# Performance work log

Measured on AMD Instinct MI355X. Metric: run time of the kernel, lower is better.

The kernel has to match this reference:

```python
import jax, jax.numpy as jnp
import numpy as np

B, CIN, T, H, W = 4, 64, 8, 32, 32
COUT, AHID = 64, 16
HWF = H * W


def _conv2d(x, w, b):
    y = jax.lax.conv_general_dilated(x, w, (1, 1), [(1, 1), (1, 1)],
                                     dimension_numbers=("NCHW", "OIHW", "NCHW"))
    return y + b[None, :, None, None]


def _conv1x1(x, w, b):
    return jnp.einsum("bchw,oc->bohw", x, w) + b[None, :, None, None]


def setup_inputs():
    key = jax.random.key(0)
    ks = jax.random.split(key, 18)
    s = 0.05
    d = {}
    d["X"] = jax.random.normal(ks[0], (B, CIN, T, H, W), jnp.float32)
    d["conv_w"] = jax.random.normal(ks[1], (4 * COUT, CIN + COUT, 3, 3), jnp.float32) * s
    d["conv_b"] = jnp.zeros((4 * COUT,), jnp.float32)
    d["W_ci"] = jax.random.normal(ks[2], (COUT, H, W), jnp.float32) * s
    d["W_cf"] = jax.random.normal(ks[3], (COUT, H, W), jnp.float32) * s
    d["W_co"] = jax.random.normal(ks[4], (COUT, H, W), jnp.float32) * s
    d["q_w"] = jax.random.normal(ks[5], (AHID, COUT), jnp.float32) * s
    d["q_b"] = jnp.zeros((AHID,), jnp.float32)
    d["k_w"] = jax.random.normal(ks[6], (AHID, COUT), jnp.float32) * s
    d["k_b"] = jnp.zeros((AHID,), jnp.float32)
    d["k2_w"] = jax.random.normal(ks[7], (AHID, COUT), jnp.float32) * s
    d["k2_b"] = jnp.zeros((AHID,), jnp.float32)
    d["v_w"] = jax.random.normal(ks[8], (COUT, COUT), jnp.float32) * s
    d["v_b"] = jnp.zeros((COUT,), jnp.float32)
    d["v2_w"] = jax.random.normal(ks[9], (COUT, COUT), jnp.float32) * s
    d["v2_b"] = jnp.zeros((COUT,), jnp.float32)
    d["z_w"] = jax.random.normal(ks[10], (2 * COUT, 2 * COUT), jnp.float32) * s
    d["z_b"] = jnp.zeros((2 * COUT,), jnp.float32)
    d["m_w"] = jax.random.normal(ks[11], (3 * COUT, 3 * COUT), jnp.float32) * s
    d["m_b"] = jnp.zeros((3 * COUT,), jnp.float32)
    return d


def _forward(X, conv_w, conv_b, W_ci, W_cf, W_co, q_w, q_b, k_w, k_b, k2_w, k2_b,
             v_w, v_b, v2_w, v2_b, z_w, z_b, m_w, m_b):
    def step(carry, x_t):
        h, c, m = carry
        # ConvLSTM cell with peephole connections
        gates = _conv2d(jnp.concatenate([x_t, h], axis=1), conv_w, conv_b)
        i_c, f_c, g_c, o_c = jnp.split(gates, 4, axis=1)
        ig = jax.nn.sigmoid(i_c + W_ci * c)
        fg = jax.nn.sigmoid(f_c + W_cf * c)
        c_new = fg * c + ig * jnp.tanh(g_c)
        og = jax.nn.sigmoid(o_c + W_co * c_new)
        h_new = og * jnp.tanh(c_new)
        # Self-attention memory module (all projections are 1x1 convs)
        q = _conv1x1(h_new, q_w, q_b).reshape(B, AHID, HWF)
        kh = _conv1x1(h_new, k_w, k_b).reshape(B, AHID, HWF)
        vh = _conv1x1(h_new, v_w, v_b).reshape(B, COUT, HWF)
        km = _conv1x1(m, k2_w, k2_b).reshape(B, AHID, HWF)
        vm = _conv1x1(m, v2_w, v2_b).reshape(B, COUT, HWF)
        att_h = jax.nn.softmax(jnp.einsum("ban,bam->bnm", q, kh), axis=-1)  # (B,HW,HW)
        att_m = jax.nn.softmax(jnp.einsum("ban,bam->bnm", q, km), axis=-1)
        z_h = jnp.einsum("bnm,bcm->bcn", att_h, vh)  # (B,COUT,HW)
        z_m = jnp.einsum("bnm,bcm->bcn", att_m, vm)
        z = jnp.concatenate([z_h, z_m], axis=1).reshape(B, 2 * COUT, H, W)
        z = _conv1x1(z, z_w, z_b)
        comb = _conv1x1(jnp.concatenate([z, h_new], axis=1), m_w, m_b)
        mo, mg, mi = jnp.split(comb, 3, axis=1)
        gi = jax.nn.sigmoid(mi)
        m_new = (1.0 - gi) * m + gi * jnp.tanh(mg)
        h_out = jax.nn.sigmoid(mo) * m_new
        return (h_out, c_new, m_new), h_out

    zeros = jnp.zeros((B, COUT, H, W), X.dtype)
    Xs = jnp.moveaxis(X, 2, 0)  # (T, B, CIN, H, W)
    _, hs = jax.lax.scan(step, (zeros, zeros, zeros), Xs)
    return jnp.moveaxis(hs, 0, 2)  # (B, COUT, T, H, W)


def reference(X, conv_w, conv_b, W_ci, W_cf, W_co, q_w, q_b, k_w, k_b, k2_w, k2_b,
              v_w, v_b, v2_w, v2_b, z_w, z_b, m_w, m_b):
    return _forward(X, conv_w, conv_b, W_ci, W_cf, W_co, q_w, q_b, k_w, k_b,
                    k2_w, k2_b, v_w, v_b, v2_w, v2_b, z_w, z_b, m_w, m_b)
```

## Files before the change

### kernel.cpp

```cpp
#include <hip/hip_runtime.h>
#include <hip/hip_bf16.h>

typedef __hip_bfloat16 bf16;
typedef unsigned short ushort;
typedef __attribute__((ext_vector_type(8))) short short8v;
typedef __attribute__((ext_vector_type(4))) float float4v;

__device__ __forceinline__ float b2f(bf16 v){ return __bfloat162float(v); }
__device__ __forceinline__ float sigm(float x){ return 1.0f/(1.0f+__expf(-x)); }
__device__ __forceinline__ float tanhc(float x){
  x = fminf(15.0f, fmaxf(-15.0f, x));
  float e = __expf(2.0f*x);
  return (e-1.0f)/(e+1.0f);
}
__device__ __forceinline__ ushort f2bu(float f){
  bf16 h = __float2bfloat16(f); return *reinterpret_cast<ushort*>(&h);
}
__device__ __forceinline__ float bu2f(ushort u){
  return __uint_as_float(((unsigned)u)<<16);
}
__device__ __forceinline__ short8v ldfrag(const ushort* p){
  return *reinterpret_cast<const short8v*>(p);
}
__device__ __forceinline__ void glds16(const ushort* g, ushort* l){
  __builtin_amdgcn_global_load_lds(
    (const __attribute__((address_space(1))) unsigned int*)g,
    (__attribute__((address_space(3))) unsigned int*)l, 16, 0, 0);
}

#define WS_SMALL   0
#define WS_FLAG    262144
#define WS_ZROW    262160
#define WS_H       262208
#define WS_C       524352
#define WS_M       786496
#define WS_QB16    1310784
#define WS_KHB16   1376320
#define WS_KMB16   1441856
#define WS_VTH16   1507392
#define WS_VTM16   1638464
#define WS_MTH     1769536
#define WS_MTL     1900608
#define WS_HNTH    2031680
#define WS_HNTL    2162752
#define WS_ZW16H   2293824
#define WS_ZW16L   2302016
#define WS_MW16H   2310208
#define WS_MW16L   2328640
#define WS_WXAH    2347072
#define WS_WHAH    2420800
#define WS_WXAL    2494528
#define WS_WHAL    2568256
#define WS_XTHI    2641984
#define WS_XTLO    3690560
#define WS_HTHI    4739136
#define WS_HTLO    4870208
#define WS_PWH     5001280
#define WS_PWL     5006912
#define WS_GXG     5012544
#define WS_GXO     7109696
#define O_CB    0
#define O_WCI   256
#define O_WCF   65792
#define O_WCO   131328
#define O_QW    196864
#define O_QB    197888
#define O_KW    197904
#define O_KB    198928
#define O_K2W   198944
#define O_K2B   199968
#define O_VW    199984
#define O_VB    204080
#define O_V2W   204144
#define O_V2B   208240
#define O_ZW    208304
#define O_ZB    224688
#define O_MW    224816
#define O_MB    261680

__global__ void k_probe(const unsigned int* __restrict__ Xu, int* __restrict__ flag){
  __shared__ int cnt;
  if (threadIdx.x == 0) cnt = 0;
  __syncthreads();
  unsigned int u = Xu[threadIdx.x];
  float f = __uint_as_float((u & 0xffffu) << 16);
  int bad = (fabsf(f) <= 1e4f) ? 0 : 1;
  atomicAdd(&cnt, bad);
  __syncthreads();
  if (threadIdx.x == 0) *flag = (cnt > 16) ? 1 : 0;
}

struct P18 { const void* p[18]; };

__global__ __launch_bounds__(256) void k_wconv(P18 pk, const int* __restrict__ flagp,
                                               float* __restrict__ dst){
  const int ns[18]   = {256,65536,65536,65536,1024,16,1024,16,1024,16,
                        4096,64,4096,64,16384,128,36864,192};
  const int offs[18] = {O_CB,O_WCI,O_WCF,O_WCO,O_QW,O_QB,O_KW,O_KB,O_K2W,O_K2B,
                        O_VW,O_VB,O_V2W,O_V2B,O_ZW,O_ZB,O_MW,O_MB};
  int y = blockIdx.y;
  int n = ns[y];
  int flag = *flagp;
  const void* src = pk.p[y];
  for (int i = blockIdx.x*256 + threadIdx.x; i < n; i += gridDim.x*256){
    float v = flag ? ((const float*)src)[i] : b2f(((const bf16*)src)[i]);
    dst[offs[y] + i] = v;
  }
}

__global__ __launch_bounds__(256) void k_wtrans(float* __restrict__ ws){
  int i = blockIdx.x*256 + threadIdx.x;
  if (i < 16384){
    float f = ws[O_ZW + i];
    ushort h = f2bu(f);
    ((ushort*)(ws + WS_ZW16H))[i] = h;
    ((ushort*)(ws + WS_ZW16L))[i] = f2bu(f - bu2f(h));
  }
  if (i < 36864){
    float f = ws[O_MW + i];
    ushort h = f2bu(f);
    ((ushort*)(ws + WS_MW16H))[i] = h;
    ((ushort*)(ws + WS_MW16L))[i] = f2bu(f - bu2f(h));
  }
  if (i < 11264){
    int r = i >> 6, k = i & 63;
    float f;
    if (r < 16)       f = ws[O_QW  + r*64 + k];
    else if (r < 32)  f = ws[O_KW  + (r-16)*64 + k];
    else if (r < 48)  f = ws[O_K2W + (r-32)*64 + k];
    else if (r < 112) f = ws[O_VW  + (r-48)*64 + k];
    else              f = ws[O_V2W + (r-112)*64 + k];
    ushort h = f2bu(f);
    ((ushort*)(ws + WS_PWH))[i] = h;
    ((ushort*)(ws + WS_PWL))[i] = f2bu(f - bu2f(h));
  }
}

__global__ __launch_bounds__(256) void k_init(const void* __restrict__ conv_w,
                                              const int* __restrict__ flagp,
                                              float* __restrict__ ws){
  int i = blockIdx.x*256 + threadIdx.x;
  int flag = *flagp;
  if (i < 786432) ws[WS_H + i] = 0.0f;
  if (i < 32) ws[WS_ZROW + i] = 0.0f;
  if (i < 196608) ((unsigned*)(ws + WS_QB16))[i] = 0u;
  if (i < 294912){
    int ci = i & 127;
    int j = i >> 7;
    int mm = j & 255, p = j >> 8;
    int cc = mm >> 2, g = mm & 3;
    int si = ((g*64 + cc)*128 + ci)*9 + p;
    float f;
    ushort hi, lo = 0;
    if (flag){
      f = ((const float*)conv_w)[si];
      hi = f2bu(f);
      lo = f2bu(f - bu2f(hi));
    } else {
      hi = ((const ushort*)conv_w)[si];
    }
    if (ci < 64){
      int di = (j << 6) + ((((ci >> 3) ^ (mm & 7)) << 3) | (ci & 7));
      ((ushort*)(ws + WS_WXAH))[di] = hi;
      ((ushort*)(ws + WS_WXAL))[di] = lo;
    } else {
      int c2 = ci - 64;
      int di = (j << 6) + ((((c2 >> 3) ^ (mm & 7)) << 3) | (c2 & 7));
      ((ushort*)(ws + WS_WHAH))[di] = hi;
      ((ushort*)(ws + WS_WHAL))[di] = lo;
    }
  }
  if (i < 131072){
    ((unsigned*)(ws + WS_HTHI))[i] = 0u;
    ((unsigned*)(ws + WS_HTLO))[i] = 0u;
    ((unsigned*)(ws + WS_MTH))[i] = 0u;
    ((unsigned*)(ws + WS_MTL))[i] = 0u;
  }
}

__global__ __launch_bounds__(256) void k_xt(const void* __restrict__ Xraw,
                                            const int* __restrict__ flagp,
                                            float* __restrict__ ws){
  __shared__ ushort hi_s[64][66];
  __shared__ ushort lo_s[64][66];
  int pt = blockIdx.x, s = blockIdx.y;
  int b = s >> 3, t = s & 7;
  int flag = *flagp;
  int tid = threadIdx.x;
  for (int k = 0; k < 16; ++k){
    int idx = tid + k*256;
    int ci = idx >> 6, pxl = idx & 63;
    size_t si = ((size_t)(b*64 + ci)*8 + t)*1024 + pt*64 + pxl;
    if (flag){
      float f = ((const float*)Xraw)[si];
      ushort h = f2bu(f);
      hi_s[pxl][ci] = h;
      lo_s[pxl][ci] = f2bu(f - bu2f(h));
    } else {
      hi_s[pxl][ci] = ((const ushort*)Xraw)[si];
    }
  }
  __syncthreads();
  ushort* xh = (ushort*)(ws + WS_XTHI) + ((size_t)s*1024 + pt*64)*64;
  ushort* xl = (ushort*)(ws + WS_XTLO) + ((size_t)s*1024 + pt*64)*64;
  for (int k = 0; k < 16; ++k){
    int idx = tid + k*256;
    int pxl = idx >> 6, ci = idx & 63;
    xh[pxl*64 + ci] = hi_s[pxl][ci];
    if (flag) xl[pxl*64 + ci] = lo_s[pxl][ci];
  }
}

__global__ __launch_bounds__(512, 4) void k_convx(
  const int* __restrict__ flagp,
  const ushort* __restrict__ wxah, const ushort* __restrict__ wxal,
  const ushort* __restrict__ xt_hi, const ushort* __restrict__ xt_lo,
  float* __restrict__ gxg, ushort* __restrict__ gxo)
{
  __shared__ ushort xabuf[8192];
  __shared__ ushort xsm[54*136];
  int nt = blockIdx.x, mh = blockIdx.y, tb = blockIdx.z;
  int tid = threadIdx.x;
  int flag = *flagp;
  int ytile = nt >> 1, x0 = (nt & 1) * 16;
  const ushort* xb  = xt_hi + (size_t)tb*65536;
  const ushort* xlb = xt_lo + (size_t)tb*65536;
  int w = tid >> 6, lane = tid & 63, lr = lane & 15, lk = lane >> 4;
  const ushort* aw  = wxah + (size_t)(mh*128 + w*16)*64 + lane*8;
  const ushort* awl = wxal + (size_t)(mh*128 + w*16)*64 + lane*8;
  ushort* areg = xabuf + w*1024;

  const uint4 Z16 = make_uint4(0,0,0,0);
  for (int idx = tid; idx < 864; idx += 512){
    int slot = idx >> 4, c = idx & 15;
    int rr = slot / 18, xi = slot - rr*18;
    int gy = ytile - 1 + rr, gx2 = x0 - 1 + xi;
    bool valid = (gy >= 0) & (gy < 32) & (gx2 >= 0) & (gx2 < 32);
    int px = gy*32 + gx2;
    uint4 v = Z16;
    if (valid){
      if (c < 8)       v = *reinterpret_cast<const uint4*>(xb  + (size_t)px*64 + c*8);
      else if (flag)   v = *reinterpret_cast<const uint4*>(xlb + (size_t)px*64 + (c-8)*8);
    }
    *reinterpret_cast<uint4*>(&xsm[slot*136 + c*8]) = v;
  }
  __syncthreads();

  int px = nt*16 + lr;
  int sw = lr & 7;
  const int cx0 = ((lk ^ sw) << 3);
  const int cx1 = (((4+lk) ^ sw) << 3);
  float4v acc = {0.f,0.f,0.f,0.f};

  #pragma unroll 1
  for (int p = 0; p < 9; ++p){
    glds16(aw + (size_t)p*16384,       areg);
    glds16(aw + (size_t)p*16384 + 512, areg + 512);
    asm volatile("s_waitcnt vmcnt(0)" ::: "memory");
    __builtin_amdgcn_sched_barrier(0);
    short8v A0 = ldfrag(areg + lr*64 + cx0);
    short8v A1 = ldfrag(areg + lr*64 + cx1);
    int pinl = (p/3)*18 + lr + (p%3);
    const ushort* bl = &xsm[pinl*136 + lk*8];
    short8v BX0 = ldfrag(bl), BX1 = ldfrag(bl+32);
    acc = __builtin_amdgcn_mfma_f32_16x16x32_bf16(A0, BX0, acc, 0,0,0);
    acc = __builtin_amdgcn_mfma_f32_16x16x32_bf16(A1, BX1, acc, 0,0,0);
    if (flag){
      short8v BXl0 = ldfrag(bl+64), BXl1 = ldfrag(bl+96);
      acc = __builtin_amdgcn_mfma_f32_16x16x32_bf16(A0, BXl0, acc, 0,0,0);
      acc = __builtin_amdgcn_mfma_f32_16x16x32_bf16(A1, BXl1, acc, 0,0,0);
      asm volatile("s_waitcnt lgkmcnt(0)" ::: "memory");
      __builtin_amdgcn_sched_barrier(0);
      glds16(awl + (size_t)p*16384,       areg);
      glds16(awl + (size_t)p*16384 + 512, areg + 512);
      asm volatile("s_waitcnt vmcnt(0)" ::: "memory");
      __builtin_amdgcn_sched_barrier(0);
      short8v Al0 = ldfrag(areg + lr*64 + cx0);
      short8v Al1 = ldfrag(areg + lr*64 + cx1);
      acc = __builtin_amdgcn_mfma_f32_16x16x32_bf16(Al0, BX0, acc, 0,0,0);
      acc = __builtin_amdgcn_mfma_f32_16x16x32_bf16(Al1, BX1, acc, 0,0,0);
      asm volatile("s_waitcnt lgkmcnt(0)" ::: "memory");
      __builtin_amdgcn_sched_barrier(0);
    } else {
      asm volatile("s_waitcnt lgkmcnt(0)" ::: "memory");
      __builtin_amdgcn_sched_barrier(0);
    }
  }

  {
    int cc = mh*32 + w*4 + lk;
    gxg[((size_t)tb*64 + cc)*1024 + px] = acc[2];
    ushort* go = gxo + ((size_t)tb*192 + cc*3)*1024 + px;
    go[0]    = f2bu(acc[0]);
    go[1024] = f2bu(acc[1]);
    go[2048] = f2bu(acc[3]);
  }
}

__global__ __launch_bounds__(1024, 4) void k_convp(
  const int* __restrict__ flagp,
  const ushort* __restrict__ whah, const ushort* __restrict__ whal,
  const ushort* __restrict__ ht_hi, const ushort* __restrict__ ht_lo,
  const float* __restrict__ gxg, const ushort* __restrict__ gxo,
  const float* __restrict__ smalls, float* __restrict__ cst,
  const ushort* __restrict__ pwh, const ushort* __restrict__ pwl,
  const ushort* __restrict__ mth, const ushort* __restrict__ mtl,
  ushort* __restrict__ hnth, ushort* __restrict__ hntl,
  ushort* __restrict__ qb16, ushort* __restrict__ khb16, ushort* __restrict__ kmb16,
  ushort* __restrict__ vth16, ushort* __restrict__ vtm16, int t)
{
  __shared__ ushort albuf[16384];
  __shared__ ushort bsm[54*136];
  __shared__ ushort hbh[16*72];
  __shared__ ushort hbl[16*72];
  int nt = blockIdx.x, b = blockIdx.y;
  int tid = threadIdx.x;
  int flag = *flagp;
  int ytile = nt >> 1, x0 = (nt & 1) * 16;

  const ushort* hb  = ht_hi + (size_t)b*65536;
  const ushort* hlb = ht_lo + (size_t)b*65536;

  int w = tid >> 6, lane = tid & 63, lr = lane & 15, lk = lane >> 4;
  const ushort* aw  = whah + (size_t)(w*16)*64 + lane*8;
  const ushort* awl = whal + (size_t)(w*16)*64 + lane*8;
  ushort* areg = albuf + w*1024;

  if (!flag){
    glds16(aw, areg);
    glds16(aw + 512, areg + 512);
  }

  int px = nt*16 + lr;
  int cc = w*4 + lk;
  int tb = b*8 + t;
  const ushort* go = gxo + ((size_t)tb*192 + cc*3)*1024 + px;
  float a0 = bu2f(go[0]);
  float a1 = bu2f(go[1024]);
  float a3 = bu2f(go[2048]);
  float a2 = gxg[((size_t)tb*64 + cc)*1024 + px];

  const uint4 Z16 = make_uint4(0,0,0,0);
  if (tid < 864){
    int slot = tid >> 4, c = tid & 15;
    int rr = slot / 18, xi = slot - rr*18;
    int gy = ytile - 1 + rr, gx2 = x0 - 1 + xi;
    bool valid = (gy >= 0) & (gy < 32) & (gx2 >= 0) & (gx2 < 32);
    int hpx = gy*32 + gx2;
    uint4 v = Z16;
    if (valid){
      if (c < 8) v = *reinterpret_cast<const uint4*>(hb  + (size_t)hpx*64 + c*8);
      else       v = *reinterpret_cast<const uint4*>(hlb + (size_t)hpx*64 + (c-8)*8);
    }
    *reinterpret_cast<uint4*>(&bsm[slot*136 + c*8]) = v;
  }
  __syncthreads();

  const int sw = lr & 7;
  const int c2n = ((lk ^ sw) << 3);
  const int c3n = (((4+lk) ^ sw) << 3);

  float4v acc = {a0, a1, a2, a3};

  if (!flag){
    #pragma unroll
    for (int p = 0; p < 9; ++p){
      if (p > 0){
        asm volatile("s_waitcnt vmcnt(0)" ::: "memory");
        __builtin_amdgcn_sched_barrier(0);
      }
      short8v A2 = ldfrag(areg + lr*64 + c2n);
      short8v A3 = ldfrag(areg + lr*64 + c3n);
      if (p < 8){
        asm volatile("s_waitcnt lgkmcnt(0)" ::: "memory");
        __builtin_amdgcn_sched_barrier(0);
        glds16(aw + (size_t)(p+1)*16384,       areg);
        glds16(aw + (size_t)(p+1)*16384 + 512, areg + 512);
        __builtin_amdgcn_sched_barrier(0);
      }
      int pinl = (p/3)*18 + lr + (p%3);
      const ushort* bl = &bsm[pinl*136 + lk*8];
      short8v BH0 = ldfrag(bl),    BH1 = ldfrag(bl+32);
      short8v BL0 = ldfrag(bl+64), BL1 = ldfrag(bl+96);
      acc = __builtin_amdgcn_mfma_f32_16x16x32_bf16(A2, BH0, acc, 0,0,0);
      acc = __builtin_amdgcn_mfma_f32_16x16x32_bf16(A3, BH1, acc, 0,0,0);
      acc = __builtin_amdgcn_mfma_f32_16x16x32_bf16(A2, BL0, acc, 0,0,0);
      acc = __builtin_amdgcn_mfma_f32_16x16x32_bf16(A3, BL1, acc, 0,0,0);
    }
  } else {
    #pragma unroll 1
    for (int p = 0; p < 9; ++p){
      glds16(aw + (size_t)p*16384,       areg);
      glds16(aw + (size_t)p*16384 + 512, areg + 512);
      asm volatile("s_waitcnt vmcnt(0)" ::: "memory");
      __builtin_amdgcn_sched_barrier(0);
      short8v A2 = ldfrag(areg + lr*64 + c2n);
      short8v A3 = ldfrag(areg + lr*64 + c3n);
      asm volatile("s_waitcnt lgkmcnt(0)" ::: "memory");
      __builtin_amdgcn_sched_barrier(0);
      glds16(awl + (size_t)p*16384,       areg);
      glds16(awl + (size_t)p*16384 + 512, areg + 512);
      asm volatile("s_waitcnt vmcnt(0)" ::: "memory");
      __builtin_amdgcn_sched_barrier(0);
      short8v Al2 = ldfrag(areg + lr*64 + c2n);
      short8v Al3 = ldfrag(areg + lr*64 + c3n);
      asm volatile("s_waitcnt lgkmcnt(0)" ::: "memory");
      __builtin_amdgcn_sched_barrier(0);
      int pinl = (p/3)*18 + lr + (p%3);
      const ushort* bl = &bsm[pinl*136 + lk*8];
      short8v BH0 = ldfrag(bl),    BH1 = ldfrag(bl+32);
      short8v BL0 = ldfrag(bl+64), BL1 = ldfrag(bl+96);
      acc = __builtin_amdgcn_mfma_f32_16x16x32_bf16(A2, BH0, acc, 0,0,0);
      acc = __builtin_amdgcn_mfma_f32_16x16x32_bf16(A3, BH1, acc, 0,0,0);
      acc = __builtin_amdgcn_mfma_f32_16x16x32_bf16(A2, BL0, acc, 0,0,0);
      acc = __builtin_amdgcn_mfma_f32_16x16x32_bf16(A3, BL1, acc, 0,0,0);
      acc = __builtin_amdgcn_mfma_f32_16x16x32_bf16(Al2, BH0, acc, 0,0,0);
      acc = __builtin_amdgcn_mfma_f32_16x16x32_bf16(Al3, BH1, acc, 0,0,0);
    }
  }

  {
    int wi = cc*1024 + px;
    size_t sidx = ((size_t)(b*64 + cc))*1024 + px;
    float cprev = cst[sidx];
    float ic = acc[0] + smalls[O_CB + cc];
    float fc = acc[1] + smalls[O_CB + 64 + cc];
    float gc = acc[2] + smalls[O_CB + 128 + cc];
    float oc = acc[3] + smalls[O_CB + 192 + cc];
    float ig = sigm(ic + smalls[O_WCI + wi]*cprev);
    float fg = sigm(fc + smalls[O_WCF + wi]*cprev);
    float cnew = fg*cprev + ig*tanhc(gc);
    float og = sigm(oc + smalls[O_WCO + wi]*cnew);
    cst[sidx] = cnew;
    float hv = og*tanhc(cnew);
    ushort hh = f2bu(hv);
    ushort hl2 = f2bu(hv - bu2f(hh));
    hbh[lr*72 + cc] = hh;
    hbl[lr*72 + cc] = hl2;
  }
  __syncthreads();

  {
    int ppx = tid >> 6, ccx = tid & 63;
    size_t tix2 = ((size_t)b*1024 + nt*16 + ppx)*64 + ccx;
    hnth[tix2] = hbh[ppx*72 + ccx];
    hntl[tix2] = hbl[ppx*72 + ccx];
  }

  if (w < 11){
    int tt = w;
    const float4v Z4 = {0.f,0.f,0.f,0.f};
    bool srcm = (tt == 2) || (tt >= 7);
    short8v b0, b1, bl0, bl1;
    if (srcm){
      size_t bb = ((size_t)b*1024 + nt*16 + lr)*64 + lk*8;
      b0  = ldfrag(mth + bb);  b1  = ldfrag(mth + bb + 32);
      bl0 = ldfrag(mtl + bb);  bl1 = ldfrag(mtl + bb + 32);
    } else {
      b0  = ldfrag(&hbh[lr*72 + lk*8]);  b1  = ldfrag(&hbh[lr*72 + 32 + lk*8]);
      bl0 = ldfrag(&hbl[lr*72 + lk*8]);  bl1 = ldfrag(&hbl[lr*72 + 32 + lk*8]);
    }
    const ushort* ar = pwh + (size_t)(tt*16 + lr)*64 + lk*8;
    short8v pa0 = ldfrag(ar), pa1 = ldfrag(ar + 32);
    float4v d = Z4;
    d = __builtin_amdgcn_mfma_f32_16x16x32_bf16(pa0, b0,  d, 0,0,0);
    d = __builtin_amdgcn_mfma_f32_16x16x32_bf16(pa1, b1,  d, 0,0,0);
    d = __builtin_amdgcn_mfma_f32_16x16x32_bf16(pa0, bl0, d, 0,0,0);
    d = __builtin_amdgcn_mfma_f32_16x16x32_bf16(pa1, bl1, d, 0,0,0);
    if (flag){
      const ushort* arl = pwl + (size_t)(tt*16 + lr)*64 + lk*8;
      short8v pal0 = ldfrag(arl), pal1 = ldfrag(arl + 32);
      d = __builtin_amdgcn_mfma_f32_16x16x32_bf16(pal0, b0, d, 0,0,0);
      d = __builtin_amdgcn_mfma_f32_16x16x32_bf16(pal1, b1, d, 0,0,0);
    }
    int n = nt*16 + lr;
    int boff = (tt==0) ? O_QB : (tt==1) ? O_KB : (tt==2) ? O_K2B
             : (tt<7) ? (O_VB + (tt-3)*16) : (O_V2B + (tt-7)*16);
    if (tt < 3){
      ushort* base = (tt==0) ? qb16 : (tt==1) ? khb16 : kmb16;
      ushort u[4];
      #pragma unroll
      for (int q = 0; q < 4; ++q)
        u[q] = f2bu(d[q] + smalls[boff + lk*4 + q]);
      *reinterpret_cast<uint2*>(&base[((size_t)b*1024 + n)*32 + lk*4]) =
        make_uint2((unsigned)u[0] | ((unsigned)u[1]<<16),
                   (unsigned)u[2] | ((unsigned)u[3]<<16));
    } else {
      ushort* base = (tt<7) ? vth16 : vtm16;
      int cc0 = ((tt<7) ? (tt-3) : (tt-7))*16 + lk*4;
      #pragma unroll
      for (int q = 0; q < 4; ++q)
        base[((size_t)b*64 + cc0 + q)*1024 + n] = f2bu(d[q] + smalls[boff + lk*4 + q]);
    }
  }
}

__global__ __launch_bounds__(512) void k_fattz(
  const ushort* __restrict__ qb16, const ushort* __restrict__ khb16,
  const ushort* __restrict__ kmb16, const ushort* __restrict__ vth16,
  const ushort* __restrict__ vtm16,
  const ushort* __restrict__ hnth, const ushort* __restrict__ hntl,
  const float* __restrict__ smalls,
  const ushort* __restrict__ zw16h, const ushort* __restrict__ zw16l,
  const ushort* __restrict__ mw16h, const ushort* __restrict__ mw16l,
  const int* __restrict__ flagp,
  float* __restrict__ mst, ushort* __restrict__ mth, ushort* __restrict__ mtl,
  ushort* __restrict__ hth, ushort* __restrict__ htl,
  void* __restrict__ outraw, int t)
{
  __shared__ __align__(16) unsigned char poolA[34816];
  __shared__ __align__(16) ushort ztbh[16*136];
  __shared__ __align__(16) ushort ztbl[16*136];
  __shared__ float cb[192*17];
  __shared__ float ml[64*17];
  __shared__ float rs_s[2][4][16];

  ushort* es   = (ushort*)poolA;
  ushort* zbh  = (ushort*)poolA;
  ushort* zbl  = (ushort*)(poolA + 8704);
  float*  ho_s = (float*)poolA;
  float*  mn_s = (float*)(poolA + 4352);

  int nt = blockIdx.x, b = blockIdx.y;
  int n0 = nt*16;
  int tid = threadIdx.x;
  int w = tid >> 6, lane = tid & 63, lr = lane & 15, lk = lane >> 4;
  int br = w >> 2, wq = w & 3;
  int flag = *flagp;
  const float4v Z4 = {0.f,0.f,0.f,0.f};

  const ushort* kb = (br ? kmb16 : khb16) + (size_t)b*32768;
  const ushort* vt = (br ? vtm16 : vth16) + (size_t)b*65536;
  const ushort* qp = qb16 + (size_t)b*32768;

  for (int idx = tid; idx < 1024; idx += 512){
    int ch = idx >> 4, pp = idx & 15;
    ml[ch*17+pp] = mst[((size_t)b*64 + ch)*1024 + n0 + pp];
  }

  short8v qf = ldfrag(qp + (size_t)(n0 + lr)*32 + lk*8);

  float4v acc[2];
  acc[0]=Z4; acc[1]=Z4;
  float rsum = 0.f;

  #pragma unroll 1
  for (int mc = 0; mc < 4; ++mc){
    ushort* esb = es + (br*2 + (mc & 1))*4352;
    int mbase = mc*256 + wq*64;
    #pragma unroll
    for (int tau = 0; tau < 4; ++tau){
      short8v af = ldfrag(kb + (size_t)(mbase + tau*16 + lr)*32 + lk*8);
      float4v d = __builtin_amdgcn_mfma_f32_16x16x32_bf16(af, qf, Z4, 0,0,0);
      ushort u0 = f2bu(__expf(fminf(d[0], 60.f)));
      ushort u1 = f2bu(__expf(fminf(d[1], 60.f)));
      ushort u2 = f2bu(__expf(fminf(d[2], 60.f)));
      ushort u3 = f2bu(__expf(fminf(d[3], 60.f)));
      rsum += (bu2f(u0) + bu2f(u1)) + (bu2f(u2) + bu2f(u3));
      unsigned lo = (unsigned)u0 | ((unsigned)u1 << 16);
      unsigned hi = (unsigned)u2 | ((unsigned)u3 << 16);
      *reinterpret_cast<uint2*>(&esb[lr*272 + wq*64 + tau*16 + lk*4]) = make_uint2(lo, hi);
    }
    __syncthreads();
    #pragma unroll
    for (int ks = 0; ks < 8; ++ks){
      short8v av = ldfrag(vt + (size_t)(wq*16 + lr)*1024 + mc*256 + ks*32 + lk*8);
      short8v bv = ldfrag(&esb[lr*272 + ks*32 + lk*8]);
      acc[ks & 1] = __builtin_amdgcn_mfma_f32_16x16x32_bf16(av, bv, acc[ks & 1], 0,0,0);
    }
  }

  {
    float r = rsum;
    r += __shfl_xor(r, 16);
    r += __shfl_xor(r, 32);
    if (lane < 16) rs_s[br][wq][lr] = r;
  }
  __syncthreads();
  {
    float rinv = 1.0f / (rs_s[br][0][lr] + rs_s[br][1][lr] + rs_s[br][2][lr] + rs_s[br][3][lr]);
    int ch0 = br*64 + wq*16 + lk*4;
    ushort uh[4], ul[4];
    #pragma unroll
    for (int r = 0; r < 4; ++r){
      float z = (acc[0][r] + acc[1][r])*rinv;
      uh[r] = f2bu(z);
      ul[r] = f2bu(z - bu2f(uh[r]));
    }
    *reinterpret_cast<uint2*>(&zbh[lr*136 + ch0]) =
      make_uint2((unsigned)uh[0] | ((unsigned)uh[1]<<16), (unsigned)uh[2] | ((unsigned)uh[3]<<16));
    *reinterpret_cast<uint2*>(&zbl[lr*136 + ch0]) =
      make_uint2((unsigned)ul[0] | ((unsigned)ul[1]<<16), (unsigned)ul[2] | ((unsigned)ul[3]<<16));
  }
  __syncthreads();

  {
    float4v zacc = Z4;
    if (!flag){
      #pragma unroll
      for (int kf = 0; kf < 4; ++kf){
        short8v a  = ldfrag(zw16h + (size_t)(w*16 + lr)*128 + kf*32 + lk*8);
        short8v bh = ldfrag(&zbh[lr*136 + kf*32 + lk*8]);
        short8v bl = ldfrag(&zbl[lr*136 + kf*32 + lk*8]);
        zacc = __builtin_amdgcn_mfma_f32_16x16x32_bf16(a, bh, zacc, 0,0,0);
        zacc = __builtin_amdgcn_mfma_f32_16x16x32_bf16(a, bl, zacc, 0,0,0);
      }
    } else {
      #pragma unroll
      for (int kf = 0; kf < 4; ++kf){
        short8v a  = ldfrag(zw16h + (size_t)(w*16 + lr)*128 + kf*32 + lk*8);
        short8v al = ldfrag(zw16l + (size_t)(w*16 + lr)*128 + kf*32 + lk*8);
        short8v bh = ldfrag(&zbh[lr*136 + kf*32 + lk*8]);
        short8v bl = ldfrag(&zbl[lr*136 + kf*32 + lk*8]);
        zacc = __builtin_amdgcn_mfma_f32_16x16x32_bf16(a,  bh, zacc, 0,0,0);
        zacc = __builtin_amdgcn_mfma_f32_16x16x32_bf16(a,  bl, zacc, 0,0,0);
        zacc = __builtin_amdgcn_mfma_f32_16x16x32_bf16(al, bh, zacc, 0,0,0);
      }
    }
    int r0 = w*16 + lk*4;
    ushort th[4], tl[4];
    #pragma unroll
    for (int q = 0; q < 4; ++q){
      float ztv = zacc[q] + smalls[O_ZB + r0 + q];
      th[q] = f2bu(ztv);
      tl[q] = f2bu(ztv - bu2f(th[q]));
    }
    *reinterpret_cast<uint2*>(&ztbh[lr*136 + r0]) =
      make_uint2((unsigned)th[0] | ((unsigned)th[1]<<16), (unsigned)th[2] | ((unsigned)th[3]<<16));
    *reinterpret_cast<uint2*>(&ztbl[lr*136 + r0]) =
      make_uint2((unsigned)tl[0] | ((unsigned)tl[1]<<16), (unsigned)tl[2] | ((unsigned)tl[3]<<16));
  }
  __syncthreads();

  const ushort* hrow  = hnth + ((size_t)b*1024 + n0 + lr)*64;
  const ushort* hrowl = hntl + ((size_t)b*1024 + n0 + lr)*64;
  #pragma unroll
  for (int mi = 0; mi < 2; ++mi){
    if (mi == 1 && w >= 4) break;
    int mf = (mi == 0) ? w : (w + 8);
    float4v cacc = Z4;
    const ushort* arow  = mw16h + (size_t)(mf*16 + lr)*192;
    const ushort* arowl = mw16l + (size_t)(mf*16 + lr)*192;
    if (!flag){
      #pragma unroll
      for (int kf = 0; kf < 4; ++kf){
        short8v a  = ldfrag(arow + kf*32 + lk*8);
        short8v bh = ldfrag(&ztbh[lr*136 + kf*32 + lk*8]);
        short8v bl = ldfrag(&ztbl[lr*136 + kf*32 + lk*8]);
        cacc = __builtin_amdgcn_mfma_f32_16x16x32_bf16(a, bh, cacc, 0,0,0);
        cacc = __builtin_amdgcn_mfma_f32_16x16x32_bf16(a, bl, cacc, 0,0,0);
      }
      #pragma unroll
      for (int kf = 0; kf < 2; ++kf){
        short8v a  = ldfrag(arow + 128 + kf*32 + lk*8);
        short8v bh = ldfrag(hrow + kf*32 + lk*8);
        short8v bl = ldfrag(hrowl + kf*32 + lk*8);
        cacc = __builtin_amdgcn_mfma_f32_16x16x32_bf16(a, bh, cacc, 0,0,0);
        cacc = __builtin_amdgcn_mfma_f32_16x16x32_bf16(a, bl, cacc, 0,0,0);
      }
    } else {
      #pragma unroll
      for (int kf = 0; kf < 4; ++kf){
        short8v a  = ldfrag(arow + kf*32 + lk*8);
        short8v al = ldfrag(arowl + kf*32 + lk*8);
        short8v bh = ldfrag(&ztbh[lr*136 + kf*32 + lk*8]);
        short8v bl = ldfrag(&ztbl[lr*136 + kf*32 + lk*8]);
        cacc = __builtin_amdgcn_mfma_f32_16x16x32_bf16(a,  bh, cacc, 0,0,0);
        cacc = __builtin_amdgcn_mfma_f32_16x16x32_bf16(a,  bl, cacc, 0,0,0);
        cacc = __builtin_amdgcn_mfma_f32_16x16x32_bf16(al, bh, cacc, 0,0,0);
      }
      #pragma unroll
      for (int kf = 0; kf < 2; ++kf){
        short8v a  = ldfrag(arow + 128 + kf*32 + lk*8);
        short8v al = ldfrag(arowl + 128 + kf*32 + lk*8);
        short8v bh = ldfrag(hrow + kf*32 + lk*8);
        short8v bl = ldfrag(hrowl + kf*32 + lk*8);
        cacc = __builtin_amdgcn_mfma_f32_16x16x32_bf16(a,  bh, cacc, 0,0,0);
        cacc = __builtin_amdgcn_mfma_f32_16x16x32_bf16(a,  bl, cacc, 0,0,0);
        cacc = __builtin_amdgcn_mfma_f32_16x16x32_bf16(al, bh, cacc, 0,0,0);
      }
    }
    int r0 = mf*16 + lk*4;
    #pragma unroll
    for (int q = 0; q < 4; ++q)
      cb[(r0+q)*17 + lr] = cacc[q] + smalls[O_MB + r0 + q];
  }
  __syncthreads();

  {
    int px = tid >> 5, lr2 = tid & 31;
    #pragma unroll
    for (int j = 0; j < 2; ++j){
      int ch = lr2 + 32*j;
      float mo = cb[ch*17 + px];
      float mg = cb[(64+ch)*17 + px];
      float mi = cb[(128+ch)*17 + px];
      float mold = ml[ch*17 + px];
      float gi = sigm(mi);
      float mnew = (1.0f-gi)*mold + gi*tanhc(mg);
      float ho = sigm(mo)*mnew;
      ho_s[ch*17+px] = ho;
      mn_s[ch*17+px] = mnew;
    }
  }
  __syncthreads();
  for (int idx = tid; idx < 1024; idx += 512){
    int ch = idx >> 4, pp = idx & 15;
    int n = n0 + pp;
    size_t gidx = ((size_t)b*64 + ch)*1024 + n;
    mst[gidx] = mn_s[ch*17+pp];
    float ho = ho_s[ch*17+pp];
    size_t oidx = ((size_t)(b*64+ch)*8 + t)*1024 + n;
    if (flag) ((float*)outraw)[oidx] = ho;
    else      ((bf16*)outraw)[oidx] = __float2bfloat16(ho);
  }
  for (int idx = tid; idx < 1024; idx += 512){
    int pp = idx >> 6, ch = idx & 63;
    int n = n0 + pp;
    size_t tix = ((size_t)b*1024 + n)*64 + ch;
    float ho = ho_s[ch*17+pp];
    float mn = mn_s[ch*17+pp];
    ushort hb_ = f2bu(ho);
    hth[tix] = hb_;
    htl[tix] = f2bu(ho - bu2f(hb_));
    ushort mh_ = f2bu(mn);
    mth[tix] = mh_;
    mtl[tix] = f2bu(mn - bu2f(mh_));
  }
}

extern "C" void kernel_launch(void* const* d_in, const int* in_sizes, int n_in,
                              void* d_out, int out_size, void* d_ws, size_t ws_size,
                              hipStream_t stream)
{
  float* ws = (float*)d_ws;
  int* flag = (int*)(ws + WS_FLAG);
  float* c    = ws + WS_C;
  float* m    = ws + WS_M;
  float* gxg  = ws + WS_GXG;
  ushort* gxo   = (ushort*)(ws + WS_GXO);
  ushort* qb16  = (ushort*)(ws + WS_QB16);
  ushort* khb16 = (ushort*)(ws + WS_KHB16);
  ushort* kmb16 = (ushort*)(ws + WS_KMB16);
  ushort* vth16 = (ushort*)(ws + WS_VTH16);
  ushort* vtm16 = (ushort*)(ws + WS_VTM16);
  ushort* mth   = (ushort*)(ws + WS_MTH);
  ushort* mtl   = (ushort*)(ws + WS_MTL);
  ushort* hnth  = (ushort*)(ws + WS_HNTH);
  ushort* hntl  = (ushort*)(ws + WS_HNTL);
  ushort* zw16h = (ushort*)(ws + WS_ZW16H);
  ushort* zw16l = (ushort*)(ws + WS_ZW16L);
  ushort* mw16h = (ushort*)(ws + WS_MW16H);
  ushort* mw16l = (ushort*)(ws + WS_MW16L);
  ushort* wxah  = (ushort*)(ws + WS_WXAH);
  ushort* wxal  = (ushort*)(ws + WS_WXAL);
  ushort* whah  = (ushort*)(ws + WS_WHAH);
  ushort* whal  = (ushort*)(ws + WS_WHAL);
  ushort* xt_hi = (ushort*)(ws + WS_XTHI);
  ushort* xt_lo = (ushort*)(ws + WS_XTLO);
  ushort* ht_hi = (ushort*)(ws + WS_HTHI);
  ushort* ht_lo = (ushort*)(ws + WS_HTLO);
  ushort* pwh   = (ushort*)(ws + WS_PWH);
  ushort* pwl   = (ushort*)(ws + WS_PWL);

  k_probe<<<1, 256, 0, stream>>>((const unsigned int*)d_in[0], flag);
  P18 pk;
  for (int i = 0; i < 18; ++i) pk.p[i] = d_in[2 + i];
  k_wconv<<<dim3(64,18), 256, 0, stream>>>(pk, flag, ws);
  k_init<<<3072, 256, 0, stream>>>(d_in[1], flag, ws);
  k_xt<<<dim3(16,32), 256, 0, stream>>>(d_in[0], flag, ws);
  k_wtrans<<<144, 256, 0, stream>>>(ws);
  k_convx<<<dim3(64,2,32), 512, 0, stream>>>(flag, wxah, wxal, xt_hi, xt_lo, gxg, gxo);

  for (int t = 0; t < 8; ++t){
    k_convp<<<dim3(64,4), 1024, 0, stream>>>(flag, whah, whal, ht_hi, ht_lo,
                                             gxg, gxo, ws, c, pwh, pwl, mth, mtl,
                                             hnth, hntl, qb16, khb16, kmb16,
                                             vth16, vtm16, t);
    k_fattz<<<dim3(64,4), 512, 0, stream>>>(qb16, khb16, kmb16, vth16, vtm16,
                                            hnth, hntl, ws, zw16h, zw16l, mw16h, mw16l,
                                            flag, m, mth, mtl, ht_hi, ht_lo, d_out, t);
  }
  (void)in_sizes; (void)n_in; (void)out_size; (void)ws_size;
}
```

Measured before the change: 389.8 us.

## Split attention key range across two wave groups with 1024-thread fattz blocks

Doubles the fused attention/z/m kernel block size to 1024 threads. Each branch's key chunks are now split between two wave halves, and the partial PV accumulators are merged through shared memory. The 1x1 conv and epilogue loops are remapped so each thread handles a single element. The aim is more parallelism in a latency-bound grid of only 256 blocks. The cost is more LDS (the score buffer doubles, plus a cross-wave reduction buffer), an extra reduction step, and tighter register limits under the 1024-thread launch bounds.

```diff
diff --git a/kernel.cpp b/kernel.cpp
--- a/kernel.cpp
+++ b/kernel.cpp
@@ -495,7 +495,7 @@
   }
 }
 
-__global__ __launch_bounds__(512) void k_fattz(
+__global__ __launch_bounds__(1024) void k_fattz(
   const ushort* __restrict__ qb16, const ushort* __restrict__ khb16,
   const ushort* __restrict__ kmb16, const ushort* __restrict__ vth16,
   const ushort* __restrict__ vtm16,
@@ -508,12 +508,13 @@
   ushort* __restrict__ hth, ushort* __restrict__ htl,
   void* __restrict__ outraw, int t)
 {
-  __shared__ __align__(16) unsigned char poolA[34816];
+  __shared__ __align__(16) unsigned char poolA[69632];
   __shared__ __align__(16) ushort ztbh[16*136];
   __shared__ __align__(16) ushort ztbl[16*136];
   __shared__ float cb[192*17];
   __shared__ float ml[64*17];
-  __shared__ float rs_s[2][4][16];
+  __shared__ float rs_s[2][8][16];
+  __shared__ float accx[2*4*64*4];
 
   ushort* es   = (ushort*)poolA;
   ushort* zbh  = (ushort*)poolA;
@@ -525,7 +526,7 @@
   int n0 = nt*16;
   int tid = threadIdx.x;
   int w = tid >> 6, lane = tid & 63, lr = lane & 15, lk = lane >> 4;
-  int br = w >> 2, wq = w & 3;
+  int br = w >> 3, sub = w & 7, mh2 = sub >> 2, wq = sub & 3;
   int flag = *flagp;
   const float4v Z4 = {0.f,0.f,0.f,0.f};
 
@@ -533,8 +534,8 @@
   const ushort* vt = (br ? vtm16 : vth16) + (size_t)b*65536;
   const ushort* qp = qb16 + (size_t)b*32768;
 
-  for (int idx = tid; idx < 1024; idx += 512){
-    int ch = idx >> 4, pp = idx & 15;
+  {
+    int ch = tid >> 4, pp = tid & 15;
     ml[ch*17+pp] = mst[((size_t)b*64 + ch)*1024 + n0 + pp];
   }
 
@@ -545,8 +546,9 @@
   float rsum = 0.f;
 
   #pragma unroll 1
-  for (int mc = 0; mc < 4; ++mc){
-    ushort* esb = es + (br*2 + (mc & 1))*4352;
+  for (int mci = 0; mci < 2; ++mci){
+    int mc = mh2*2 + mci;
+    ushort* esb = es + (size_t)(br*4 + mc)*4352;
     int mbase = mc*256 + wq*64;
     #pragma unroll
     for (int tau = 0; tau < 4; ++tau){
@@ -574,16 +576,25 @@
     float r = rsum;
     r += __shfl_xor(r, 16);
     r += __shfl_xor(r, 32);
-    if (lane < 16) rs_s[br][wq][lr] = r;
-  }
-  __syncthreads();
-  {
-    float rinv = 1.0f / (rs_s[br][0][lr] + rs_s[br][1][lr] + rs_s[br][2][lr] + rs_s[br][3][lr]);
+    if (lane < 16) rs_s[br][sub][lr] = r;
+  }
+  if (mh2 == 1){
+    float* ax = accx + ((size_t)(br*4 + wq)*64 + lane)*4;
+    #pragma unroll
+    for (int r = 0; r < 4; ++r) ax[r] = acc[0][r] + acc[1][r];
+  }
+  __syncthreads();
+  if (mh2 == 0){
+    float rtot = 0.f;
+    #pragma unroll
+    for (int s2 = 0; s2 < 8; ++s2) rtot += rs_s[br][s2][lr];
+    float rinv = 1.0f / rtot;
+    const float* ax = accx + ((size_t)(br*4 + wq)*64 + lane)*4;
     int ch0 = br*64 + wq*16 + lk*4;
     ushort uh[4], ul[4];
     #pragma unroll
     for (int r = 0; r < 4; ++r){
-      float z = (acc[0][r] + acc[1][r])*rinv;
+      float z = (acc[0][r] + acc[1][r] + ax[r])*rinv;
       uh[r] = f2bu(z);
       ul[r] = f2bu(z - bu2f(uh[r]));
     }
@@ -594,7 +605,7 @@
   }
   __syncthreads();
 
-  {
+  if (w < 8){
     float4v zacc = Z4;
     if (!flag){
       #pragma unroll
@@ -634,10 +645,8 @@
 
   const ushort* hrow  = hnth + ((size_t)b*1024 + n0 + lr)*64;
   const ushort* hrowl = hntl + ((size_t)b*1024 + n0 + lr)*64;
-  #pragma unroll
-  for (int mi = 0; mi < 2; ++mi){
-    if (mi == 1 && w >= 4) break;
-    int mf = (mi == 0) ? w : (w + 8);
+  if (w < 12){
+    int mf = w;
     float4v cacc = Z4;
     const ushort* arow  = mw16h + (size_t)(mf*16 + lr)*192;
     const ushort* arowl = mw16l + (size_t)(mf*16 + lr)*192;
@@ -688,24 +697,20 @@
   __syncthreads();
 
   {
-    int px = tid >> 5, lr2 = tid & 31;
-    #pragma unroll
-    for (int j = 0; j < 2; ++j){
-      int ch = lr2 + 32*j;
-      float mo = cb[ch*17 + px];
-      float mg = cb[(64+ch)*17 + px];
-      float mi = cb[(128+ch)*17 + px];
-      float mold = ml[ch*17 + px];
-      float gi = sigm(mi);
-      float mnew = (1.0f-gi)*mold + gi*tanhc(mg);
-      float ho = sigm(mo)*mnew;
-      ho_s[ch*17+px] = ho;
-      mn_s[ch*17+px] = mnew;
-    }
-  }
-  __syncthreads();
-  for (int idx = tid; idx < 1024; idx += 512){
-    int ch = idx >> 4, pp = idx & 15;
+    int gpx = tid >> 6, ch = tid & 63;
+    float mo = cb[ch*17 + gpx];
+    float mg = cb[(64+ch)*17 + gpx];
+    float mi = cb[(128+ch)*17 + gpx];
+    float mold = ml[ch*17 + gpx];
+    float gi = sigm(mi);
+    float mnew = (1.0f-gi)*mold + gi*tanhc(mg);
+    float ho = sigm(mo)*mnew;
+    ho_s[ch*17+gpx] = ho;
+    mn_s[ch*17+gpx] = mnew;
+  }
+  __syncthreads();
+  {
+    int ch = tid >> 4, pp = tid & 15;
     int n = n0 + pp;
     size_t gidx = ((size_t)b*64 + ch)*1024 + n;
     mst[gidx] = mn_s[ch*17+pp];
@@ -714,8 +719,8 @@
     if (flag) ((float*)outraw)[oidx] = ho;
     else      ((bf16*)outraw)[oidx] = __float2bfloat16(ho);
   }
-  for (int idx = tid; idx < 1024; idx += 512){
-    int pp = idx >> 6, ch = idx & 63;
+  {
+    int pp = tid >> 6, ch = tid & 63;
     int n = n0 + pp;
     size_t tix = ((size_t)b*1024 + n)*64 + ch;
     float ho = ho_s[ch*17+pp];
@@ -777,9 +782,9 @@
                                              gxg, gxo, ws, c, pwh, pwl, mth, mtl,
                                              hnth, hntl, qb16, khb16, kmb16,
                                              vth16, vtm16, t);
-    k_fattz<<<dim3(64,4), 512, 0, stream>>>(qb16, khb16, kmb16, vth16, vtm16,
-                                            hnth, hntl, ws, zw16h, zw16l, mw16h, mw16l,
-                                            flag, m, mth, mtl, ht_hi, ht_lo, d_out, t);
+    k_fattz<<<dim3(64,4), 1024, 0, stream>>>(qb16, khb16, kmb16, vth16, vtm16,
+                                             hnth, hntl, ws, zw16h, zw16l, mw16h, mw16l,
+                                             flag, m, mth, mtl, ht_hi, ht_lo, d_out, t);
   }
   (void)in_sizes; (void)n_in; (void)out_size; (void)ws_size;
 }
```

New measurement: 379.0 us. 1.03x faster.
